# Kernel tuning notes

Measured on AMD Instinct MI355X. Metric: run time of the kernel, lower is better.

Reference implementation:

```python
import jax, jax.numpy as jnp
import numpy as np
from jax import lax

V_TH = 1.0    # base firing threshold
RHO = 0.9     # adaptive-threshold decay
ADAPT = 0.1   # threshold increment per spike
SLOPE = 5.0   # surrogate-gradient sigmoid slope

@jax.custom_vjp
def spike_fn(v):
    return (v >= 0.0).astype(v.dtype)

def _spike_fwd(v):
    return spike_fn(v), v

def _spike_bwd(v, g):
    s = jax.nn.sigmoid(SLOPE * v)
    return (g * SLOPE * s * (1.0 - s),)

spike_fn.defvjp(_spike_fwd, _spike_bwd)

def lif_scan(x_seq, beta):
    # x_seq: (T, ..., F) channel-last; beta: (F,). Adaptive LIF with soft reset.
    def step(carry, x):
        mem, b = carry
        mem = beta * mem + x
        th = V_TH + b
        spk = spike_fn(mem - th)
        mem = mem - spk * th
        b = RHO * b + ADAPT * spk
        return (mem, b), spk
    z = jnp.zeros_like(x_seq[0])
    _, spikes = lax.scan(step, (z, z), x_seq)
    return spikes

def conv2d_s2(x, w, b):
    # NCHW conv, stride 2, padding 1
    y = lax.conv_general_dilated(x, w, (2, 2), ((1, 1), (1, 1)),
                                 dimension_numbers=('NCHW', 'OIHW', 'NCHW'))
    return y + b[None, :, None, None]

def mha(x, wq, wk, wv, wo, nh=4):
    B, T, D = x.shape
    dh = D // nh
    q = (x @ wq.T).reshape(B, T, nh, dh)
    k = (x @ wk.T).reshape(B, T, nh, dh)
    v = (x @ wv.T).reshape(B, T, nh, dh)
    att = jnp.einsum('bqhd,bkhd->bhqk', q, k) * (dh ** -0.5)
    p = jax.nn.softmax(att, axis=-1)
    o = jnp.einsum('bhqk,bkhd->bqhd', p, v).reshape(B, T, D)
    return o @ wo.T

def _forward(x, conv1_w, conv1_b, conv2_w, conv2_b, beta1, beta2,
             proj_w, proj_b, wq, wk, wv, wo, cls_w, cls_b):
    B, T, C, H, W = x.shape
    H1, W1, H2, W2 = H // 2, W // 2, H // 4, W // 4
    # stage 1 conv over all timesteps at once (conv is stateless)
    c1 = conv2d_s2(x.reshape(B * T, C, H, W), conv1_w, conv1_b)       # (B*T,16,H1,W1)
    c1 = jnp.moveaxis(c1.reshape(B, T, 16, H1, W1), 2, -1)            # (B,T,H1,W1,16)
    c1 = jnp.moveaxis(c1, 1, 0)                                       # (T,B,H1,W1,16)
    s1 = lif_scan(c1, beta1)                                          # (T,B,H1,W1,16)
    s1 = jnp.moveaxis(jnp.moveaxis(s1, 0, 1), -1, 2)                  # (B,T,16,H1,W1)
    # stage 2
    c2 = conv2d_s2(s1.reshape(B * T, 16, H1, W1), conv2_w, conv2_b)   # (B*T,32,H2,W2)
    c2 = jnp.moveaxis(c2.reshape(B, T, 32, H2, W2), 2, -1)
    c2 = jnp.moveaxis(c2, 1, 0)                                       # (T,B,H2,W2,32)
    s2 = lif_scan(c2, beta2)                                          # (T,B,H2,W2,32)
    total_spikes = s2.sum()
    # flatten channel-major to match torch permute(0,3,1,2).view(B,-1)
    feats = jnp.moveaxis(s2, -1, 2)                                   # (T,B,32,H2,W2)
    feats = jnp.moveaxis(feats, 0, 1).reshape(B, T, -1)               # (B,T,32*H2*W2)
    proj = feats @ proj_w.T + proj_b                                  # (B,T,64)
    attn = mha(proj, wq, wk, wv, wo)                                  # (B,T,64)
    context = attn.mean(axis=1)                                       # (B,64)
    # lif_out single step from zero state: mem = context
    spk_out = spike_fn(context - V_TH)
    logits = spk_out @ cls_w.T + cls_b
    sparsity = 1.0 - total_spikes / float(feats.size)
    return logits, sparsity

def setup_inputs() -> dict:
    key = jax.random.key(0)
    ks = jax.random.split(key, 10)
    B, T, C, H, W = 64, 8, 2, 128, 128
    D = 64
    flat = 32 * (H // 4) * (W // 4)  # 32768
    f = jnp.float32
    return {
        'x': (jax.random.uniform(ks[0], (B, T, C, H, W)) < 0.1).astype(f),  # sparse DVS events
        'conv1_w': jax.random.normal(ks[1], (16, C, 3, 3), f) * 0.2,
        'conv1_b': jnp.zeros((16,), f),
        'conv2_w': jax.random.normal(ks[2], (32, 16, 3, 3), f) * 0.1,
        'conv2_b': jnp.zeros((32,), f),
        'beta1': jnp.full((16,), 0.9, f),
        'beta2': jnp.full((32,), 0.9, f),
        'proj_w': jax.random.normal(ks[3], (D, flat), f) * (flat ** -0.5),
        'proj_b': jnp.zeros((D,), f),
        'wq': jax.random.normal(ks[4], (D, D), f) * (D ** -0.5),
        'wk': jax.random.normal(ks[5], (D, D), f) * (D ** -0.5),
        'wv': jax.random.normal(ks[6], (D, D), f) * (D ** -0.5),
        'wo': jax.random.normal(ks[7], (D, D), f) * (D ** -0.5),
        'cls_w': jax.random.normal(ks[8], (2, D), f) * (D ** -0.5),
        'cls_b': jnp.zeros((2,), f),
    }

def reference(x, conv1_w, conv1_b, conv2_w, conv2_b, beta1, beta2,
              proj_w, proj_b, wq, wk, wv, wo, cls_w, cls_b):
    return _forward(x, conv1_w, conv1_b, conv2_w, conv2_b, beta1, beta2,
                    proj_w, proj_b, wq, wk, wv, wo, cls_w, cls_b)
```

## Files before the change

kernel.cpp:

```cpp
#include <hip/hip_runtime.h>
#include <cstdint>

#define V_TH 1.0f
#define RHO 0.9f
#define ADAPT 0.1f

static constexpr int B = 64, T = 8, C = 2, H = 128, W = 128;
static constexpr int H1 = 64, W1 = 64;
static constexpr int H2 = 32, W2 = 32;
static constexpr int FLAT = 32 * H2 * W2;
static constexpr int R = B * T;

static constexpr size_t OFF_TRIP  = 0;
static constexpr size_t OFF_BITS  = OFF_TRIP + 8388608;
static constexpr size_t OFF_PWT   = OFF_BITS + 2097152;
static constexpr size_t OFF_CNT   = OFF_PWT + 8388608;
static constexpr size_t OFF_TBL   = OFF_CNT + 256;
static constexpr size_t OFF_PART  = OFF_TBL + 6291456;

__global__ __launch_bounds__(256) void k_mega1(
    const float* __restrict__ x, const float* __restrict__ w,
    const float* __restrict__ bias, const float* __restrict__ beta,
    uint64_t* __restrict__ trip,
    const float* __restrict__ pw, float* __restrict__ pwt,
    const float* __restrict__ c2w, float* __restrict__ tbl,
    unsigned int* __restrict__ cnt) {
  __shared__ float shmem[64 * 65];
  int bid = blockIdx.x;
  int tid = threadIdx.x;
  if (bid < 1024) {
    float* sw1 = shmem;
    for (int i = tid; i < 288; i += 256) {
      int c = i / 18, j = i % 18;
      sw1[j * 68 + c] = w[i];
    }
    __syncthreads();
    int gid = bid * 256 + tid;
    int w1 = gid & 63, h1 = (gid >> 6) & 63, b = gid >> 12;
    int lane = tid & 63;
    float bias_r[16], beta_r[16];
#pragma unroll
    for (int c = 0; c < 16; ++c) { bias_r[c] = bias[c]; beta_r[c] = beta[c]; }
    float mem[16], bth[16];
#pragma unroll
    for (int c = 0; c < 16; ++c) { mem[c] = 0.f; bth[c] = 0.f; }
    for (int t = 0; t < T; ++t) {
      int r = b * T + t;
      const float* xb = x + (size_t)(r * 2) * 16384;
      uint32_t M = 0;
#pragma unroll
      for (int ci = 0; ci < 2; ++ci) {
#pragma unroll
        for (int kh = 0; kh < 3; ++kh) {
          int y = 2 * h1 - 1 + kh;
          uint32_t w3 = 0;
          if (y >= 0 && y < H) {
            float2 v = *(const float2*)(xb + ci * 16384 + y * 128 + 2 * lane);
            float nl = __shfl(v.y, lane - 1, 64);
            uint32_t bl = (lane > 0 && nl != 0.f) ? 1u : 0u;
            uint32_t bm = (v.x != 0.f) ? 2u : 0u;
            uint32_t br = (v.y != 0.f) ? 4u : 0u;
            w3 = bl | bm | br;
          }
          M |= w3 << ((ci * 3 + kh) * 3);
        }
      }
      float acc[16];
#pragma unroll
      for (int c = 0; c < 16; ++c) acc[c] = bias_r[c];
      while (M) {
        int j = __ffs(M) - 1; M &= M - 1;
        const float4* wr = (const float4*)&sw1[j * 68];
        float4 a0 = wr[0], a1 = wr[1], a2 = wr[2], a3 = wr[3];
        acc[0] += a0.x; acc[1] += a0.y; acc[2] += a0.z; acc[3] += a0.w;
        acc[4] += a1.x; acc[5] += a1.y; acc[6] += a1.z; acc[7] += a1.w;
        acc[8] += a2.x; acc[9] += a2.y; acc[10] += a2.z; acc[11] += a2.w;
        acc[12] += a3.x; acc[13] += a3.y; acc[14] += a3.z; acc[15] += a3.w;
      }
      uint32_t mask = 0;
#pragma unroll
      for (int c = 0; c < 16; ++c) {
        mem[c] = beta_r[c] * mem[c] + acc[c];
        float th = V_TH + bth[c];
        bool s = (mem[c] >= th);
        if (s) { mem[c] -= th; mask |= (1u << c); }
        bth[c] = RHO * bth[c] + (s ? ADAPT : 0.f);
      }
      int iL = 2 * lane - 1; if (iL < 0) iL = 0;
      uint32_t mL = __shfl((int)mask, iL, 64);
      uint32_t mC = __shfl((int)mask, 2 * lane, 64);
      uint32_t mR = __shfl((int)mask, 2 * lane + 1, 64);
      if (lane < 32) {
        uint64_t tw = (uint64_t)(lane ? mL : 0u) | ((uint64_t)mC << 16) |
                      ((uint64_t)mR << 32);
        trip[(size_t)(r * H1 + h1) * 32 + lane] = tw;
      }
    }
  } else if (bid < 1536) {
    float* tile = shmem;
    int tb = bid - 1024;
    int c = tb >> 4, pt = tb & 15;
    int posc = ((c & 3) << 3) + (c >> 2);
    int p0 = pt * 64;
    int lane = tid & 63, quad = tid >> 6;
#pragma unroll
    for (int it = 0; it < 16; ++it) {
      int d = it * 4 + quad;
      tile[d * 65 + lane] = pw[(size_t)d * FLAT + c * 1024 + p0 + lane];
    }
    __syncthreads();
#pragma unroll
    for (int it = 0; it < 16; ++it) {
      int pp = it * 4 + quad;
      pwt[((size_t)((p0 + pp) * 32 + posc)) * 64 + lane] = tile[lane * 65 + pp];
    }
  } else if (bid == 1536) {
    if (tid == 0) *cnt = 0u;
  } else {
    int idx = bid - 1537;
    int g = idx >> 4;
    int kh = g >> 2, gp = g & 3;
    int v = ((idx & 15) << 8) + tid;
    float e[32];
#pragma unroll
    for (int co = 0; co < 32; ++co) e[co] = 0.f;
    for (int i = 0; i < 12; ++i) {
      if ((v >> i) & 1) {
        int j = gp * 12 + i;
        int kw = j >> 4, ci = j & 15;
#pragma unroll
        for (int co = 0; co < 32; ++co)
          e[co] += c2w[((co * 16 + ci) * 3 + kh) * 3 + kw];
      }
    }
#pragma unroll
    for (int co = 0; co < 32; ++co)
      tbl[((size_t)(g * 4096 + v)) * 32 + co] = e[co];
  }
}

__global__ __launch_bounds__(256) void k_conv2_lif2(
    const uint64_t* __restrict__ trip, const float* __restrict__ tbl,
    const float* __restrict__ bias, const float* __restrict__ beta,
    uint32_t* __restrict__ bits, unsigned int* __restrict__ cnt) {
  __shared__ unsigned int sc;
  int tid = threadIdx.x;
  if (tid == 0) sc = 0u;
  __syncthreads();
  int lane = tid & 63;
  int li = lane & 7;
  int p8 = lane >> 3;
  int wvi = (blockIdx.x * 256 + tid) >> 6;
  int px = wvi * 8 + p8;
  int w2 = px & 31, h2 = (px >> 5) & 31, b = px >> 10;
  float4 b4 = *(const float4*)&bias[4 * li];
  float4 bt4 = *(const float4*)&beta[4 * li];
  float m0v = 0.f, m1v = 0.f, m2v = 0.f, m3v = 0.f;
  float t0 = 0.f, t1 = 0.f, t2 = 0.f, t3 = 0.f;
  unsigned int lc = 0;
  const float4* tb4 = (const float4*)tbl;
  for (int t = 0; t < T; ++t) {
    int r = b * T + t;
    const uint64_t* tr = trip + (size_t)(r * 64 + 2 * h2) * 32 + w2;
    uint64_t q0 = (h2 > 0) ? tr[-32] : 0ull;
    uint64_t q1 = tr[0];
    uint64_t q2 = tr[32];
    uint32_t r0l = (uint32_t)q0, r0h = (uint32_t)(q0 >> 32);
    uint32_t r1l = (uint32_t)q1, r1h = (uint32_t)(q1 >> 32);
    uint32_t r2l = (uint32_t)q2, r2h = (uint32_t)(q2 >> 32);
    float4 v0 = tb4[(0 << 15) + ((r0l & 4095u) << 3) + li];
    float4 v1 = tb4[(1 << 15) + (((r0l >> 12) & 4095u) << 3) + li];
    float4 v2 = tb4[(2 << 15) + ((((r0l >> 24) | (r0h << 8)) & 4095u) << 3) + li];
    float4 v3 = tb4[(3 << 15) + (((r0h >> 4) & 4095u) << 3) + li];
    float4 v4 = tb4[(4 << 15) + ((r1l & 4095u) << 3) + li];
    float4 v5 = tb4[(5 << 15) + (((r1l >> 12) & 4095u) << 3) + li];
    float4 v6 = tb4[(6 << 15) + ((((r1l >> 24) | (r1h << 8)) & 4095u) << 3) + li];
    float4 v7 = tb4[(7 << 15) + (((r1h >> 4) & 4095u) << 3) + li];
    float4 v8 = tb4[(8 << 15) + ((r2l & 4095u) << 3) + li];
    float4 v9 = tb4[(9 << 15) + (((r2l >> 12) & 4095u) << 3) + li];
    float4 va = tb4[(10 << 15) + ((((r2l >> 24) | (r2h << 8)) & 4095u) << 3) + li];
    float4 vb = tb4[(11 << 15) + (((r2h >> 4) & 4095u) << 3) + li];
    float A0 = b4.x + v0.x + v1.x + v2.x + v3.x;
    float A1 = b4.y + v0.y + v1.y + v2.y + v3.y;
    float A2 = b4.z + v0.z + v1.z + v2.z + v3.z;
    float A3 = b4.w + v0.w + v1.w + v2.w + v3.w;
    float B0 = v4.x + v5.x + v6.x + v7.x;
    float B1 = v4.y + v5.y + v6.y + v7.y;
    float B2 = v4.z + v5.z + v6.z + v7.z;
    float B3 = v4.w + v5.w + v6.w + v7.w;
    float C0 = v8.x + v9.x + va.x + vb.x;
    float C1 = v8.y + v9.y + va.y + vb.y;
    float C2 = v8.z + v9.z + va.z + vb.z;
    float C3 = v8.w + v9.w + va.w + vb.w;
    float a0 = (A0 + B0) + C0, a1 = (A1 + B1) + C1;
    float a2 = (A2 + B2) + C2, a3 = (A3 + B3) + C3;
    m0v = bt4.x * m0v + a0;
    m1v = bt4.y * m1v + a1;
    m2v = bt4.z * m2v + a2;
    m3v = bt4.w * m3v + a3;
    float th0 = V_TH + t0, th1 = V_TH + t1, th2 = V_TH + t2, th3 = V_TH + t3;
    bool s0 = (m0v >= th0), s1 = (m1v >= th1), s2 = (m2v >= th2), s3 = (m3v >= th3);
    if (s0) m0v -= th0;
    if (s1) m1v -= th1;
    if (s2) m2v -= th2;
    if (s3) m3v -= th3;
    t0 = RHO * t0 + (s0 ? ADAPT : 0.f);
    t1 = RHO * t1 + (s1 ? ADAPT : 0.f);
    t2 = RHO * t2 + (s2 ? ADAPT : 0.f);
    t3 = RHO * t3 + (s3 ? ADAPT : 0.f);
    unsigned long long bl0 = __ballot(s0);
    unsigned long long bl1 = __ballot(s1);
    unsigned long long bl2 = __ballot(s2);
    unsigned long long bl3 = __ballot(s3);
    if (li == 0) {
      int sh = p8 * 8;
      uint32_t m32 = ((uint32_t)(bl0 >> sh) & 0xFFu)
                   | (((uint32_t)(bl1 >> sh) & 0xFFu) << 8)
                   | (((uint32_t)(bl2 >> sh) & 0xFFu) << 16)
                   | (((uint32_t)(bl3 >> sh) & 0xFFu) << 24);
      bits[(size_t)r * 1024 + (px & 1023)] = m32;
      lc += __popc(m32);
    }
  }
  if (li == 0) atomicAdd(&sc, lc);
  __syncthreads();
  if (tid == 0) atomicAdd(cnt, sc);
}

__global__ __launch_bounds__(256) void k_proj_gemm(
    const uint32_t* __restrict__ bits, const float* __restrict__ pwt,
    float* __restrict__ partial) {
  int rt = blockIdx.x >> 4;
  int ks = (blockIdx.x & 15) * 4 + (threadIdx.x >> 6);
  int d = threadIdx.x & 63;
  float acc[8] = {0, 0, 0, 0, 0, 0, 0, 0};
  const uint32_t* bb = bits + (size_t)rt * 8 * 1024;
  for (int wi = 0; wi < 16; ++wi) {
    int word = ks * 16 + wi;
    const float* rowbase = pwt + ((size_t)word * 32) * 64 + d;
#pragma unroll
    for (int ri = 0; ri < 8; ++ri) {
      uint32_t m = bb[ri * 1024 + word];
      while (m) {
        int c = __ffs(m) - 1; m &= m - 1;
        acc[ri] += rowbase[c << 6];
      }
    }
  }
#pragma unroll
  for (int ri = 0; ri < 8; ++ri)
    partial[((size_t)(rt * 64 + ks) * 8 + ri) * 64 + d] = acc[ri];
}

__global__ __launch_bounds__(256) void k_attn_final(
    const float* __restrict__ partial, const float* __restrict__ pb,
    const float* __restrict__ wq, const float* __restrict__ wk,
    const float* __restrict__ wv, const float* __restrict__ wo,
    const float* __restrict__ clsw, const float* __restrict__ clsb,
    const unsigned int* __restrict__ cnt, float* __restrict__ out) {
  __shared__ float swq[64 * 65], swk[64 * 65], swv[64 * 65], swo[64 * 65];
  __shared__ float sp[8 * 65], sq[8 * 65], sk[8 * 65], sv[8 * 65], so2[8 * 65];
  __shared__ float satt[4][8][8];
  __shared__ float sob[64];
  int b = blockIdx.x, tid = threadIdx.x;
  for (int i = tid; i < 4096; i += 256) {
    int dd = i >> 6, e = i & 63;
    swq[dd * 65 + e] = wq[i]; swk[dd * 65 + e] = wk[i];
    swv[dd * 65 + e] = wv[i]; swo[dd * 65 + e] = wo[i];
  }
  for (int i = tid; i < 512; i += 256) {
    int ri = i >> 6, d = i & 63;
    float s = pb[d];
    const float* p = partial + ((size_t)(b * 64) * 8 + ri) * 64 + d;
#pragma unroll
    for (int ks = 0; ks < 64; ++ks) s += p[(size_t)ks * 512];
    sp[ri * 65 + d] = s;
  }
  __syncthreads();
#pragma unroll
  for (int p = 0; p < 2; ++p) {
    int idx = p * 256 + tid, t = idx >> 6, d = idx & 63;
    float qa = 0.f, ka = 0.f, va = 0.f;
    for (int e = 0; e < 64; ++e) {
      float pe = sp[t * 65 + e];
      qa += pe * swq[d * 65 + e];
      ka += pe * swk[d * 65 + e];
      va += pe * swv[d * 65 + e];
    }
    sq[t * 65 + d] = qa; sk[t * 65 + d] = ka; sv[t * 65 + d] = va;
  }
  __syncthreads();
  {
    int h = tid >> 6, q = (tid >> 3) & 7, k = tid & 7;
    float s = 0.f;
    for (int j = 0; j < 16; ++j)
      s += sq[q * 65 + h * 16 + j] * sk[k * 65 + h * 16 + j];
    satt[h][q][k] = s * 0.25f;
  }
  __syncthreads();
  if (tid < 32) {
    int h = tid >> 3, q2 = tid & 7;
    float m = -1e30f;
    for (int k2 = 0; k2 < 8; ++k2) m = fmaxf(m, satt[h][q2][k2]);
    float sum = 0.f;
    for (int k2 = 0; k2 < 8; ++k2) {
      float e = expf(satt[h][q2][k2] - m);
      satt[h][q2][k2] = e; sum += e;
    }
    float inv = 1.f / sum;
    for (int k2 = 0; k2 < 8; ++k2) satt[h][q2][k2] *= inv;
  }
  __syncthreads();
#pragma unroll
  for (int p = 0; p < 2; ++p) {
    int idx = p * 256 + tid, t = idx >> 6, d = idx & 63;
    int h = d >> 4;
    float o = 0.f;
    for (int k = 0; k < 8; ++k) o += satt[h][t][k] * sv[k * 65 + d];
    so2[t * 65 + d] = o;
  }
  __syncthreads();
  if (tid < 64) {
    float ob = 0.f;
    for (int t = 0; t < 8; ++t) ob += so2[t * 65 + tid];
    sob[tid] = ob * 0.125f;
  }
  __syncthreads();
  if (tid < 64) {
    float ctx = 0.f;
    for (int e = 0; e < 64; ++e) ctx += sob[e] * swo[tid * 65 + e];
    int spk = (ctx >= V_TH) ? 1 : 0;
    unsigned long long ball = __ballot(spk);
    if (tid < 2) {
      float lg = clsb[tid];
      for (int dd = 0; dd < 64; ++dd)
        if ((ball >> dd) & 1ull) lg += clsw[tid * 64 + dd];
      out[b * 2 + tid] = lg;
    }
    if (b == 0 && tid == 2)
      out[128] = 1.f - (float)(*cnt) / 16777216.f;
  }
}

extern "C" void kernel_launch(void* const* d_in, const int* in_sizes, int n_in,
                              void* d_out, int out_size, void* d_ws, size_t ws_size,
                              hipStream_t stream) {
  const float* x    = (const float*)d_in[0];
  const float* c1w  = (const float*)d_in[1];
  const float* c1b  = (const float*)d_in[2];
  const float* c2w  = (const float*)d_in[3];
  const float* c2b  = (const float*)d_in[4];
  const float* bt1  = (const float*)d_in[5];
  const float* bt2  = (const float*)d_in[6];
  const float* pw   = (const float*)d_in[7];
  const float* pb   = (const float*)d_in[8];
  const float* wq   = (const float*)d_in[9];
  const float* wk   = (const float*)d_in[10];
  const float* wv   = (const float*)d_in[11];
  const float* wo   = (const float*)d_in[12];
  const float* clsw = (const float*)d_in[13];
  const float* clsb = (const float*)d_in[14];
  float* out = (float*)d_out;

  uint8_t* ws = (uint8_t*)d_ws;
  uint64_t* trip  = (uint64_t*)(ws + OFF_TRIP);
  uint32_t* bits  = (uint32_t*)(ws + OFF_BITS);
  float*    pwt   = (float*)(ws + OFF_PWT);
  unsigned int* cnt = (unsigned int*)(ws + OFF_CNT);
  float*    tbl   = (float*)(ws + OFF_TBL);
  float*    part  = (float*)(ws + OFF_PART);

  k_mega1<<<1729, 256, 0, stream>>>(x, c1w, c1b, bt1, trip, pw, pwt, c2w, tbl, cnt);
  k_conv2_lif2<<<2048, 256, 0, stream>>>(trip, tbl, c2b, bt2, bits, cnt);
  k_proj_gemm<<<1024, 256, 0, stream>>>(bits, pwt, part);
  k_attn_final<<<64, 256, 0, stream>>>(part, pb, wq, wk, wv, wo, clsw, clsb, cnt, out);
}
```

Measured before the change: 215.7 us.

## Split conv1+LIF1 channels across lane pairs to double parallelism

The stage-1 conv+LIF work is now split so each output pixel is handled by two threads, each owning 8 of the 16 channels. This doubles the block count for that phase and halves the per-thread register arrays and weight loads. The spike masks of a lane pair are merged through a shuffle, staged in shared memory, and then packed into the triplet words. The cost is two extra __syncthreads per timestep, redundant input loads, and a smaller fraction of lanes doing the final writes.

```diff
diff --git a/kernel.cpp b/kernel.cpp
--- a/kernel.cpp
+++ b/kernel.cpp
@@ -28,22 +28,30 @@
   __shared__ float shmem[64 * 65];
   int bid = blockIdx.x;
   int tid = threadIdx.x;
-  if (bid < 1024) {
+  if (bid < 2048) {
     float* sw1 = shmem;
+    uint16_t* s1m = (uint16_t*)(shmem + 1280);
     for (int i = tid; i < 288; i += 256) {
       int c = i / 18, j = i % 18;
       sw1[j * 68 + c] = w[i];
     }
     __syncthreads();
-    int gid = bid * 256 + tid;
-    int w1 = gid & 63, h1 = (gid >> 6) & 63, b = gid >> 12;
+    int b = bid >> 5;
+    int rp = bid & 31;
     int lane = tid & 63;
-    float bias_r[16], beta_r[16];
-#pragma unroll
-    for (int c = 0; c < 16; ++c) { bias_r[c] = bias[c]; beta_r[c] = beta[c]; }
-    float mem[16], bth[16];
-#pragma unroll
-    for (int c = 0; c < 16; ++c) { mem[c] = 0.f; bth[c] = 0.f; }
+    int lrow = tid >> 7;
+    int half = (tid >> 6) & 1;
+    int p = lane >> 1;
+    int ch = lane & 1;
+    int h1 = rp * 2 + lrow;
+    int w1 = half * 32 + p;
+    float bias_r[8], beta_r[8];
+#pragma unroll
+    for (int c = 0; c < 8; ++c) { bias_r[c] = bias[ch * 8 + c];
+                                  beta_r[c] = beta[ch * 8 + c]; }
+    float mem[8], bth[8];
+#pragma unroll
+    for (int c = 0; c < 8; ++c) { mem[c] = 0.f; bth[c] = 0.f; }
     for (int t = 0; t < T; ++t) {
       int r = b * T + t;
       const float* xb = x + (size_t)(r * 2) * 16384;
@@ -55,9 +63,11 @@
           int y = 2 * h1 - 1 + kh;
           uint32_t w3 = 0;
           if (y >= 0 && y < H) {
-            float2 v = *(const float2*)(xb + ci * 16384 + y * 128 + 2 * lane);
-            float nl = __shfl(v.y, lane - 1, 64);
-            uint32_t bl = (lane > 0 && nl != 0.f) ? 1u : 0u;
+            const float* rowp = xb + ci * 16384 + y * 128;
+            float2 v = *(const float2*)(rowp + 2 * w1);
+            float nl = __shfl(v.y, lane - 2, 64);
+            if (p == 0) nl = (w1 > 0) ? rowp[2 * w1 - 1] : 0.f;
+            uint32_t bl = (w1 > 0 && nl != 0.f) ? 1u : 0u;
             uint32_t bm = (v.x != 0.f) ? 2u : 0u;
             uint32_t br = (v.y != 0.f) ? 4u : 0u;
             w3 = bl | bm | br;
@@ -65,40 +75,43 @@
           M |= w3 << ((ci * 3 + kh) * 3);
         }
       }
-      float acc[16];
-#pragma unroll
-      for (int c = 0; c < 16; ++c) acc[c] = bias_r[c];
+      float acc[8];
+#pragma unroll
+      for (int c = 0; c < 8; ++c) acc[c] = bias_r[c];
       while (M) {
         int j = __ffs(M) - 1; M &= M - 1;
-        const float4* wr = (const float4*)&sw1[j * 68];
-        float4 a0 = wr[0], a1 = wr[1], a2 = wr[2], a3 = wr[3];
+        const float4* wr = (const float4*)&sw1[j * 68 + ch * 8];
+        float4 a0 = wr[0], a1 = wr[1];
         acc[0] += a0.x; acc[1] += a0.y; acc[2] += a0.z; acc[3] += a0.w;
         acc[4] += a1.x; acc[5] += a1.y; acc[6] += a1.z; acc[7] += a1.w;
-        acc[8] += a2.x; acc[9] += a2.y; acc[10] += a2.z; acc[11] += a2.w;
-        acc[12] += a3.x; acc[13] += a3.y; acc[14] += a3.z; acc[15] += a3.w;
-      }
-      uint32_t mask = 0;
-#pragma unroll
-      for (int c = 0; c < 16; ++c) {
+      }
+      uint32_t mask8 = 0;
+#pragma unroll
+      for (int c = 0; c < 8; ++c) {
         mem[c] = beta_r[c] * mem[c] + acc[c];
         float th = V_TH + bth[c];
         bool s = (mem[c] >= th);
-        if (s) { mem[c] -= th; mask |= (1u << c); }
+        if (s) { mem[c] -= th; mask8 |= (1u << c); }
         bth[c] = RHO * bth[c] + (s ? ADAPT : 0.f);
       }
-      int iL = 2 * lane - 1; if (iL < 0) iL = 0;
-      uint32_t mL = __shfl((int)mask, iL, 64);
-      uint32_t mC = __shfl((int)mask, 2 * lane, 64);
-      uint32_t mR = __shfl((int)mask, 2 * lane + 1, 64);
-      if (lane < 32) {
-        uint64_t tw = (uint64_t)(lane ? mL : 0u) | ((uint64_t)mC << 16) |
-                      ((uint64_t)mR << 32);
-        trip[(size_t)(r * H1 + h1) * 32 + lane] = tw;
-      }
-    }
-  } else if (bid < 1536) {
+      uint32_t other = (uint32_t)__shfl((int)mask8, lane ^ 1, 64);
+      if (ch == 0)
+        s1m[lrow * 64 + w1] = (uint16_t)(mask8 | (other << 8));
+      __syncthreads();
+      if (tid < 64) {
+        int row = tid >> 5, w2 = tid & 31;
+        const uint16_t* sr = &s1m[row * 64];
+        uint64_t m0 = (w2 > 0) ? sr[2 * w2 - 1] : 0u;
+        uint64_t m1 = sr[2 * w2];
+        uint64_t m2 = sr[2 * w2 + 1];
+        trip[(size_t)(r * 64 + rp * 2 + row) * 32 + w2] =
+            m0 | (m1 << 16) | (m2 << 32);
+      }
+      __syncthreads();
+    }
+  } else if (bid < 2560) {
     float* tile = shmem;
-    int tb = bid - 1024;
+    int tb = bid - 2048;
     int c = tb >> 4, pt = tb & 15;
     int posc = ((c & 3) << 3) + (c >> 2);
     int p0 = pt * 64;
@@ -114,10 +127,10 @@
       int pp = it * 4 + quad;
       pwt[((size_t)((p0 + pp) * 32 + posc)) * 64 + lane] = tile[lane * 65 + pp];
     }
-  } else if (bid == 1536) {
+  } else if (bid == 2560) {
     if (tid == 0) *cnt = 0u;
   } else {
-    int idx = bid - 1537;
+    int idx = bid - 2561;
     int g = idx >> 4;
     int kh = g >> 2, gp = g & 3;
     int v = ((idx & 15) << 8) + tid;
@@ -370,7 +383,7 @@
   float*    tbl   = (float*)(ws + OFF_TBL);
   float*    part  = (float*)(ws + OFF_PART);
 
-  k_mega1<<<1729, 256, 0, stream>>>(x, c1w, c1b, bt1, trip, pw, pwt, c2w, tbl, cnt);
+  k_mega1<<<2753, 256, 0, stream>>>(x, c1w, c1b, bt1, trip, pw, pwt, c2w, tbl, cnt);
   k_conv2_lif2<<<2048, 256, 0, stream>>>(trip, tbl, c2b, bt2, bits, cnt);
   k_proj_gemm<<<1024, 256, 0, stream>>>(bits, pwt, part);
   k_attn_final<<<64, 256, 0, stream>>>(part, pb, wq, wk, wv, wo, clsw, clsb, cnt, out);
```

After: 250.4 us. 1.16x slower.
